# Kernel tuning notes

Hardware: AMD Instinct MI355X
Metric: run time of the kernel (lower is better)

## Reference

```python
import jax, jax.numpy as jnp
import numpy as np

B, T, D = 2, 2048, 1024
H, HKV, HD = 16, 4, 64  # num_heads, num_kv_heads, head_dim
EPS = 1.1920929e-07  # torch.finfo(float32).eps, nn.RMSNorm default


def _rmsnorm(x, g):
    return x * jax.lax.rsqrt(jnp.mean(x * x, axis=-1, keepdims=True) + EPS) * g


def _ternary(w):
    # ternary quantize {-1,0,+1} with straight-through estimator
    th = jnp.mean(jnp.abs(w))
    wt = jnp.sign(w) * (jnp.abs(w) > th).astype(w.dtype)
    return w + jax.lax.stop_gradient(wt - w)


def _bitlinear(x, w, g):
    return _rmsnorm(x, g) @ _ternary(w).T


def setup_inputs() -> dict:
    key = jax.random.key(0)
    ks = jax.random.split(key, 5)
    kaiming = lambda k, shape: jax.random.normal(k, shape, jnp.float32) * np.float32(np.sqrt(2.0 / shape[1]))
    return {
        "x": jax.random.normal(ks[0], (B, T, D), jnp.float32),
        "q_w": kaiming(ks[1], (D, D)),
        "q_g": jnp.ones((D,), jnp.float32),
        "k_w": kaiming(ks[2], (HKV * HD, D)),
        "k_g": jnp.ones((D,), jnp.float32),
        "v_w": kaiming(ks[3], (HKV * HD, D)),
        "o_w": kaiming(ks[4], (D, D)),
        "o_g": jnp.ones((D,), jnp.float32),
        "qk_gain": jnp.float32(5.25),
    }


def reference(x, q_w, q_g, k_w, k_g, v_w, o_w, o_g, qk_gain):
    b, t, d = x.shape
    q = _bitlinear(x, q_w, q_g).reshape(b, t, H, HD)          # [B,T,H,hd]
    k = _bitlinear(x, k_w, k_g).reshape(b, t, HKV, HD)        # [B,T,Hkv,hd]
    v = (x @ v_w.T).reshape(b, t, HKV, HD)                    # [B,T,Hkv,hd]
    rep = H // HKV
    k = jnp.repeat(k, rep, axis=2)                            # GQA expand -> [B,T,H,hd]
    v = jnp.repeat(v, rep, axis=2)
    scale = qk_gain / np.float32(np.sqrt(HD))
    attn = jnp.einsum('bqhd,bkhd->bhqk', q, k) * scale        # [B,H,T,T]
    causal = jnp.tril(jnp.ones((t, t), bool))
    attn = jnp.where(causal, attn, -jnp.inf)
    attn = jax.nn.softmax(attn, axis=-1)
    out = jnp.einsum('bhqk,bkhd->bqhd', attn, v).reshape(b, t, d)
    return _bitlinear(out, o_w, o_g)
```

## Files before the change

### kernel.cpp

```cpp
#include <hip/hip_runtime.h>
#include <hip/hip_bf16.h>
#include <cstdint>
#include <cstddef>

typedef unsigned short u16;
typedef unsigned int u32;
typedef __attribute__((ext_vector_type(8))) short short8v;
typedef __attribute__((ext_vector_type(4))) float f32x4;
typedef __attribute__((ext_vector_type(4))) u16 u16x4;
typedef __attribute__((ext_vector_type(8))) u16 u16x8;

static constexpr int Bc = 2, Tc = 2048, Dc = 1024, Hc = 16, HKVc = 4, HDc = 64;
static constexpr int Mc = Bc * Tc;
static constexpr float EPSc = 1.1920929e-07f;

static __device__ __forceinline__ u16 f2bf(float f) {
  u32 u = __builtin_bit_cast(u32, f);
  return (u16)((u + 0x7fffu + ((u >> 16) & 1u)) >> 16);
}
static __device__ __forceinline__ float bf2f(u16 b) {
  u32 u = ((u32)b) << 16;
  return __builtin_bit_cast(float, u);
}
static __device__ __forceinline__ float fast_exp2(float x) {
  float r;
  asm("v_exp_f32 %0, %1" : "=v"(r) : "v"(x));
  return r;
}
static __device__ __forceinline__ u32 cvt_pk_bf16(float lo, float hi) {
  u32 r;
  asm("v_cvt_pk_bf16_f32 %0, %1, %2" : "=v"(r) : "v"(lo), "v"(hi));
  return r;
}

__global__ __launch_bounds__(256) void np_leafsum_all(const float* __restrict__ q_w,
                                                      const float* __restrict__ k_w,
                                                      const float* __restrict__ o_w,
                                                      float* __restrict__ leaf) {
  int blk = blockIdx.x;
  const float* w;
  float* out;
  int lfbase;
  if (blk < 256)      { w = q_w; out = leaf;         lfbase = blk * 32; }
  else if (blk < 320) { w = k_w; out = leaf + 8192;  lfbase = (blk - 256) * 32; }
  else                { w = o_w; out = leaf + 10240; lfbase = (blk - 320) * 32; }
  int t = threadIdx.x;
  int lf = lfbase + (t >> 3), j = t & 7;
  const float* a = w + (size_t)lf * 128;
  float r = fabsf(a[j]);
#pragma unroll
  for (int i = 8; i < 128; i += 8) r += fabsf(a[i + j]);
  float x = r + __shfl_xor(r, 1);
  float y = x + __shfl_xor(x, 2);
  float z = y + __shfl_xor(y, 4);
  if (j == 0) out[lf] = z;
}

__global__ __launch_bounds__(256) void np_treemean3(const float* __restrict__ leaf,
                                                    float* __restrict__ th) {
  int m = blockIdx.x;
  const float* src = leaf + (m == 0 ? 0 : (m == 1 ? 8192 : 10240));
  int nle = (m == 1) ? 2048 : 8192;
  float inv_n = (m == 1) ? (1.0f / 262144.0f) : (1.0f / 1048576.0f);
  int t = threadIdx.x;
  int chunk = nle >> 8;
  float v[32];
  for (int i = 0; i < chunk; i += 4) {
    float4 f = *(const float4*)&src[t * chunk + i];
    v[i] = f.x; v[i + 1] = f.y; v[i + 2] = f.z; v[i + 3] = f.w;
  }
  for (int cnt = chunk >> 1; cnt >= 1; cnt >>= 1)
    for (int i = 0; i < cnt; ++i) v[i] = v[2 * i] + v[2 * i + 1];
  float s = v[0];
#pragma unroll
  for (int off = 1; off < 64; off <<= 1) s += __shfl_xor(s, off);
  __shared__ float red[4];
  if ((t & 63) == 0) red[t >> 6] = s;
  __syncthreads();
  if (t == 0) th[m] = ((red[0] + red[1]) + (red[2] + red[3])) * inv_n;
}

__global__ __launch_bounds__(256) void quant_split_all(const float* __restrict__ q_w,
                                                       const float* __restrict__ k_w,
                                                       const float* __restrict__ o_w,
                                                       const float* __restrict__ v_w,
                                                       const float* __restrict__ th,
                                                       u16* __restrict__ Wq,
                                                       u16* __restrict__ Wk,
                                                       u16* __restrict__ Wo,
                                                       u16* __restrict__ Vwh) {
  int i4 = blockIdx.x * 256 + threadIdx.x;
  if (i4 < 589824) {
    const float* w; u16* o; float t;
    int j;
    if (i4 < 262144)      { w = q_w; o = Wq; t = th[0]; j = i4; }
    else if (i4 < 327680) { w = k_w; o = Wk; t = th[1]; j = i4 - 262144; }
    else                  { w = o_w; o = Wo; t = th[2]; j = i4 - 327680; }
    float4 v = *(const float4*)&w[(size_t)j * 4];
    float y[4] = {v.x, v.y, v.z, v.w};
    u16x4 q;
#pragma unroll
    for (int c = 0; c < 4; ++c)
      q[c] = (y[c] > t) ? (u16)0x3F80 : ((y[c] < -t) ? (u16)0xBF80 : (u16)0);
    *(u16x4*)&o[(size_t)j * 4] = q;
  } else {
    int j = i4 - 589824;
    float4 v = *(const float4*)&v_w[(size_t)j * 4];
    float y[4] = {v.x, v.y, v.z, v.w};
    u16x4 h;
#pragma unroll
    for (int c = 0; c < 4; ++c) h[c] = f2bf(y[c]);
    *(u16x4*)&Vwh[(size_t)j * 4] = h;
  }
}

__global__ __launch_bounds__(256) void rmsnorm_split6(const float* __restrict__ X,
                                                      const float* __restrict__ g1,
                                                      const float* __restrict__ g2,
                                                      u16* __restrict__ H1, u16* __restrict__ L1,
                                                      u16* __restrict__ H2, u16* __restrict__ L2,
                                                      u16* __restrict__ HV) {
  int row = blockIdx.x;
  const float* xr = X + (size_t)row * Dc;
  int tid = threadIdx.x;
  float4 v = *(const float4*)&xr[tid * 4];
  float vv[4] = {v.x, v.y, v.z, v.w};
  if (HV != nullptr) {
    u16x4 h;
#pragma unroll
    for (int j = 0; j < 4; ++j) h[j] = f2bf(vv[j]);
    *(u16x4*)&HV[(size_t)row * Dc + tid * 4] = h;
  }
  float ss = v.x * v.x + v.y * v.y + v.z * v.z + v.w * v.w;
#pragma unroll
  for (int off = 1; off < 64; off <<= 1) ss += __shfl_xor(ss, off);
  __shared__ float red[4];
  if ((tid & 63) == 0) red[tid >> 6] = ss;
  __syncthreads();
  float tot = red[0] + red[1] + red[2] + red[3];
  float inv = 1.0f / sqrtf(tot * (1.0f / (float)Dc) + EPSc);
  {
    float4 a = *(const float4*)&g1[tid * 4];
    float ga[4] = {a.x, a.y, a.z, a.w};
    u16x4 h, l;
#pragma unroll
    for (int j = 0; j < 4; ++j) {
      float y = vv[j] * inv * ga[j];
      u16 hb = f2bf(y);
      h[j] = hb;
      l[j] = f2bf(y - bf2f(hb));
    }
    *(u16x4*)&H1[(size_t)row * Dc + tid * 4] = h;
    *(u16x4*)&L1[(size_t)row * Dc + tid * 4] = l;
  }
  {
    float4 a = *(const float4*)&g2[tid * 4];
    float ga[4] = {a.x, a.y, a.z, a.w};
    u16x4 h, l;
#pragma unroll
    for (int j = 0; j < 4; ++j) {
      float y = vv[j] * inv * ga[j];
      u16 hb = f2bf(y);
      h[j] = hb;
      l[j] = f2bf(y - bf2f(hb));
    }
    *(u16x4*)&H2[(size_t)row * Dc + tid * 4] = h;
    *(u16x4*)&L2[(size_t)row * Dc + tid * 4] = l;
  }
}

template <bool PA, int MODE>
static __device__ __forceinline__ void gemm_body(
    const u16* __restrict__ Ah, const u16* __restrict__ Al,
    const u16* __restrict__ Bh,
    int N, int K, int bm, int bn,
    float* __restrict__ C, u16* __restrict__ O1, u16* __restrict__ O2,
    u16* smem) {
  constexpr int APT = 2, BPT = 4;
  u16* AhS = smem;
  u16* AlS = smem + 4096;
  u16* BhS = smem + 8192;
  int tid = threadIdx.x;
  int l = tid & 63, w = tid >> 6;
  int wm = (w >> 1) * 32, wn = (w & 1) * 64;
  u16x8 rAh[APT], rAl[PA ? APT : 1], rBh[BPT];
  f32x4 acc[2][4] = {};
#define LOADTILE(kb_)                                                               \
  {                                                                                 \
    _Pragma("unroll") for (int p = 0; p < APT; ++p) {                               \
      int idx = tid + p * 256;                                                      \
      int row = idx >> 3, cc = idx & 7;                                             \
      rAh[p] = *(const u16x8*)&Ah[(size_t)(bm + row) * K + (kb_) + cc * 8];         \
      if (PA) rAl[p] = *(const u16x8*)&Al[(size_t)(bm + row) * K + (kb_) + cc * 8]; \
    }                                                                               \
    _Pragma("unroll") for (int p = 0; p < BPT; ++p) {                               \
      int idx = tid + p * 256;                                                      \
      int row = idx >> 3, cc = idx & 7;                                             \
      rBh[p] = *(const u16x8*)&Bh[(size_t)(bn + row) * K + (kb_) + cc * 8];         \
    }                                                                               \
  }
  LOADTILE(0)
  for (int kb = 0; kb < K; kb += 64) {
    __syncthreads();
#pragma unroll
    for (int p = 0; p < APT; ++p) {
      int idx = tid + p * 256;
      int row = idx >> 3, cc = idx & 7;
      int off = row * 64 + ((cc * 8) ^ ((row & 7) << 3));
      *(u16x8*)&AhS[off] = rAh[p];
      if (PA) *(u16x8*)&AlS[off] = rAl[p];
    }
#pragma unroll
    for (int p = 0; p < BPT; ++p) {
      int idx = tid + p * 256;
      int row = idx >> 3, cc = idx & 7;
      int off = row * 64 + ((cc * 8) ^ ((row & 7) << 3));
      *(u16x8*)&BhS[off] = rBh[p];
    }
    if (kb + 64 < K) LOADTILE(kb + 64)
    __syncthreads();
    __builtin_amdgcn_s_setprio(1);
#pragma unroll
    for (int sl = 0; sl < 2; ++sl) {
      short8v fa[2], fal[2], fb[4];
      int kof = (l >> 4) * 8 + sl * 32;
#pragma unroll
      for (int m = 0; m < 2; ++m) {
        int row = wm + m * 16 + (l & 15);
        int off = row * 64 + (kof ^ ((row & 7) << 3));
        fa[m] = *(const short8v*)&AhS[off];
        if (PA) fal[m] = *(const short8v*)&AlS[off];
      }
#pragma unroll
      for (int n = 0; n < 4; ++n) {
        int row = wn + n * 16 + (l & 15);
        int off = row * 64 + (kof ^ ((row & 7) << 3));
        fb[n] = *(const short8v*)&BhS[off];
      }
#pragma unroll
      for (int m = 0; m < 2; ++m)
#pragma unroll
        for (int n = 0; n < 4; ++n) {
          acc[m][n] = __builtin_amdgcn_mfma_f32_16x16x32_bf16(fa[m], fb[n], acc[m][n], 0, 0, 0);
          if (PA)
            acc[m][n] = __builtin_amdgcn_mfma_f32_16x16x32_bf16(fal[m], fb[n], acc[m][n], 0, 0, 0);
        }
    }
    __builtin_amdgcn_s_setprio(0);
  }
#undef LOADTILE
#pragma unroll
  for (int m = 0; m < 2; ++m)
#pragma unroll
    for (int n = 0; n < 4; ++n)
#pragma unroll
      for (int r = 0; r < 4; ++r) {
        int grow = bm + wm + m * 16 + (l >> 4) * 4 + r;
        int gcol = bn + wn + n * 16 + (l & 15);
        float v = acc[m][n][r];
        if (MODE == 0) {
          C[(size_t)grow * N + gcol] = v;
        } else if (MODE == 1) {
          u16 hb = f2bf(v);
          O1[(size_t)grow * N + gcol] = hb;
          O2[(size_t)grow * N + gcol] = f2bf(v - bf2f(hb));
        } else {
          int k = gcol & 31;
          int gp = (gcol & ~31) | (((k >> 2) & 3) << 3) |
                   (((k >> 4) & 1) << 2) | (k & 3);
          O1[(size_t)grow * N + gp] = f2bf(v);
        }
      }
}

__global__ __launch_bounds__(256, 1) void qkv_mega(
    const u16* __restrict__ Xqh, const u16* __restrict__ Xql, const u16* __restrict__ Wq,
    const u16* __restrict__ Xkh, const u16* __restrict__ Xkl, const u16* __restrict__ Wk,
    const u16* __restrict__ Xvh, const u16* __restrict__ Vwh,
    u16* __restrict__ Qh, u16* __restrict__ Ql,
    u16* __restrict__ Kh, u16* __restrict__ Kl,
    u16* __restrict__ Vt) {
  __shared__ __align__(16) u16 SMEM[16384];
  int bx = blockIdx.x;
  if (bx < 512) {
    int bm = (bx >> 3) * 64, bn = (bx & 7) * 128;
    gemm_body<true, 1>(Xqh, Xql, Wq, 1024, 1024, bm, bn, nullptr, Qh, Ql, SMEM);
  } else if (bx < 640) {
    int t = bx - 512;
    int bm = (t >> 1) * 64, bn = (t & 1) * 128;
    gemm_body<true, 1>(Xkh, Xkl, Wk, 256, 1024, bm, bn, nullptr, Kh, Kl, SMEM);
  } else {
    int t = bx - 640;
    int bm = (t >> 5) * 64, bn = (t & 31) * 128;
    gemm_body<false, 3>(Vwh, nullptr, Xvh, 4096, 1024, bm, bn, nullptr, Vt, nullptr, SMEM);
  }
}

__global__ __launch_bounds__(256, 1) void o_gemm(
    const u16* __restrict__ Ah, const u16* __restrict__ Bh,
    float* __restrict__ C) {
  __shared__ __align__(16) u16 SMEM[16384];
  int bm = blockIdx.y * 64, bn = blockIdx.x * 128;
  gemm_body<false, 0>(Ah, nullptr, Bh, 1024, 1024, bm, bn, C, nullptr, nullptr, SMEM);
}

__global__ __launch_bounds__(256, 3) void attn_part(
    const u16* __restrict__ Qh, const u16* __restrict__ Ql,
    const u16* __restrict__ Kh, const u16* __restrict__ Kl,
    const u16* __restrict__ Vt,
    const float* __restrict__ qk_gain,
    u16* __restrict__ Opart, float* __restrict__ MLpart) {
  __shared__ __align__(16) u16 SM[24576];
  int tid = threadIdx.x;
  int w = tid >> 6, l = tid & 63;
  int hb = blockIdx.x;
  int h = hb & 15, b = hb >> 4;
  int kvh = h >> 2;
  int f = blockIdx.y;
  int qt, s0, s1;
  if (f < 16) {
    qt = 15 - (f >> 1);
    int half = qt + 1;
    s0 = (f & 1) * half;
    s1 = s0 + half;
  } else {
    qt = 23 - f;
    s0 = 0;
    s1 = 2 * qt + 2;
  }
  int q0 = qt * 128;
  const float sc2 = qk_gain[0] * 0.125f * 1.44269504f;
  u16x8 pk[2], pl[2], pv[2];
#define AISSUE3(K0)                                                             \
  {                                                                             \
    _Pragma("unroll") for (int p = 0; p < 2; ++p) {                             \
      int idx = tid + p * 256;                                                  \
      int jj = idx >> 3, cc = idx & 7;                                          \
      size_t kb = ((size_t)(b * Tc + (K0) + jj)) * (HKVc * HDc) + kvh * 64 + cc * 8; \
      pk[p] = *(const u16x8*)&Kh[kb];                                           \
      pl[p] = *(const u16x8*)&Kl[kb];                                           \
      size_t vb = ((size_t)(kvh * 64 + jj)) * (size_t)Mc + b * Tc + (K0) + cc * 8; \
      pv[p] = *(const u16x8*)&Vt[vb];                                           \
    }                                                                           \
  }
#define WRITEBUF(BI)                                                            \
  {                                                                             \
    u16* bb = SM + (BI) * 12288;                                                \
    _Pragma("unroll") for (int p = 0; p < 2; ++p) {                             \
      int idx = tid + p * 256;                                                  \
      int jj = idx >> 3, cc = idx & 7;                                          \
      int sw = jj * 64 + ((cc * 8) ^ ((jj & 7) << 3));                          \
      *(u16x8*)&bb[sw] = pk[p];                                                 \
      *(u16x8*)&bb[4096 + sw] = pl[p];                                          \
      *(u16x8*)&bb[8192 + sw] = pv[p];                                          \
    }                                                                           \
  }
  short8v qb_h[4], qb_l[4];
#pragma unroll
  for (int qp = 0; qp < 2; ++qp) {
    size_t qrow = (size_t)(b * Tc + q0 + w * 32 + qp * 16 + (l & 15));
#pragma unroll
    for (int sl = 0; sl < 2; ++sl) {
      int dstart = (l >> 4) * 8 + sl * 32;
      qb_h[qp * 2 + sl] = *(const short8v*)&Qh[qrow * Dc + h * 64 + dstart];
      qb_l[qp * 2 + sl] = *(const short8v*)&Ql[qrow * Dc + h * 64 + dstart];
    }
  }
  f32x4 Oacc[8] = {{0,0,0,0},{0,0,0,0},{0,0,0,0},{0,0,0,0},
                   {0,0,0,0},{0,0,0,0},{0,0,0,0},{0,0,0,0}};
  float mrow[2] = {-3.0e38f, -3.0e38f};
  float lrow[2] = {0.f, 0.f};
  int qmax_w = q0 + w * 32 + 31;
  AISSUE3(s0 * 64)
  WRITEBUF(0)
  if (s0 + 1 < s1) AISSUE3((s0 + 1) * 64)
  __syncthreads();
  for (int li = 0; li < s1 - s0; ++li) {
    int stp = s0 + li;
    int k0 = stp * 64;
    u16* Kh_s = SM + (li & 1) * 12288;
    u16* Kl_s = Kh_s + 4096;
    u16* Vt_s = Kh_s + 8192;
    if (stp + 1 < s1) WRITEBUF((li + 1) & 1)
    if (stp + 2 < s1) AISSUE3((stp + 2) * 64)
    if (k0 <= qmax_w) {
      f32x4 s[8] = {{0,0,0,0},{0,0,0,0},{0,0,0,0},{0,0,0,0},
                    {0,0,0,0},{0,0,0,0},{0,0,0,0},{0,0,0,0}};
      __builtin_amdgcn_s_setprio(1);
#pragma unroll
      for (int kt = 0; kt < 4; ++kt) {
        int key = kt * 16 + (l & 15);
#pragma unroll
        for (int sl = 0; sl < 2; ++sl) {
          int dstart = ((l >> 4) * 8 + 32 * sl) ^ ((key & 7) << 3);
          short8v bh = *(const short8v*)&Kh_s[key * 64 + dstart];
          short8v bl = *(const short8v*)&Kl_s[key * 64 + dstart];
#pragma unroll
          for (int qp = 0; qp < 2; ++qp) {
            s[qp * 4 + kt] = __builtin_amdgcn_mfma_f32_16x16x32_bf16(bh, qb_h[qp * 2 + sl], s[qp * 4 + kt], 0, 0, 0);
            s[qp * 4 + kt] = __builtin_amdgcn_mfma_f32_16x16x32_bf16(bl, qb_h[qp * 2 + sl], s[qp * 4 + kt], 0, 0, 0);
            s[qp * 4 + kt] = __builtin_amdgcn_mfma_f32_16x16x32_bf16(bh, qb_l[qp * 2 + sl], s[qp * 4 + kt], 0, 0, 0);
          }
        }
      }
      __builtin_amdgcn_s_setprio(0);
      bool full = (k0 + 63) <= (q0 + w * 32);
      if (!full) {
#pragma unroll
        for (int qp = 0; qp < 2; ++qp) {
          int qg = q0 + w * 32 + qp * 16 + (l & 15);
#pragma unroll
          for (int kt = 0; kt < 4; ++kt)
#pragma unroll
            for (int r = 0; r < 4; ++r)
              if (k0 + kt * 16 + ((l >> 4) << 2) + r > qg) s[qp * 4 + kt][r] = -3.0e38f;
        }
      }
      float p[2][4][4];
#pragma unroll
      for (int qp = 0; qp < 2; ++qp) {
        float mk[4];
#pragma unroll
        for (int kt = 0; kt < 4; ++kt)
          mk[kt] = fmaxf(fmaxf(s[qp * 4 + kt][0], s[qp * 4 + kt][1]),
                         fmaxf(s[qp * 4 + kt][2], s[qp * 4 + kt][3]));
        float mx = fmaxf(fmaxf(mk[0], mk[1]), fmaxf(mk[2], mk[3]));
        mx = fmaxf(mx, __shfl_xor(mx, 16));
        mx = fmaxf(mx, __shfl_xor(mx, 32));
        float mnew = fmaxf(mrow[qp], mx);
        float msc = mnew * sc2;
        float corr = fast_exp2(__builtin_fmaf(mrow[qp], sc2, -msc));
        mrow[qp] = mnew;
        float sk[4];
#pragma unroll
        for (int kt = 0; kt < 4; ++kt) {
#pragma unroll
          for (int r = 0; r < 4; ++r)
            p[qp][kt][r] = fast_exp2(__builtin_fmaf(s[qp * 4 + kt][r], sc2, -msc));
          sk[kt] = (p[qp][kt][0] + p[qp][kt][1]) + (p[qp][kt][2] + p[qp][kt][3]);
        }
        float rs = (sk[0] + sk[1]) + (sk[2] + sk[3]);
        rs += __shfl_xor(rs, 16);
        rs += __shfl_xor(rs, 32);
        lrow[qp] = lrow[qp] * corr + rs;
#pragma unroll
        for (int dt = 0; dt < 4; ++dt) Oacc[qp * 4 + dt] *= corr;
      }
      short8v fbv[4];
#pragma unroll
      for (int qp = 0; qp < 2; ++qp)
#pragma unroll
        for (int sl = 0; sl < 2; ++sl) {
          union { u32 u[4]; short8v v; } fq;
          fq.u[0] = cvt_pk_bf16(p[qp][2 * sl][0], p[qp][2 * sl][1]);
          fq.u[1] = cvt_pk_bf16(p[qp][2 * sl][2], p[qp][2 * sl][3]);
          fq.u[2] = cvt_pk_bf16(p[qp][2 * sl + 1][0], p[qp][2 * sl + 1][1]);
          fq.u[3] = cvt_pk_bf16(p[qp][2 * sl + 1][2], p[qp][2 * sl + 1][3]);
          fbv[qp * 2 + sl] = fq.v;
        }
      __builtin_amdgcn_s_setprio(1);
#pragma unroll
      for (int dt = 0; dt < 4; ++dt) {
        int d = dt * 16 + (l & 15);
#pragma unroll
        for (int sl = 0; sl < 2; ++sl) {
          int kstart = ((l >> 4) * 8 + 32 * sl) ^ ((d & 7) << 3);
          short8v fav = *(const short8v*)&Vt_s[d * 64 + kstart];
#pragma unroll
          for (int qp = 0; qp < 2; ++qp)
            Oacc[qp * 4 + dt] = __builtin_amdgcn_mfma_f32_16x16x32_bf16(fav, fbv[qp * 2 + sl], Oacc[qp * 4 + dt], 0, 0, 0);
        }
      }
      __builtin_amdgcn_s_setprio(0);
    }
    __syncthreads();
  }
  int G = hb * 24 + f;
  u16* Op = Opart + (size_t)G * 8192;
  float* Es = (float*)SM + w * 1088;
#pragma unroll
  for (int qp = 0; qp < 2; ++qp) {
#pragma unroll
    for (int dt = 0; dt < 4; ++dt)
#pragma unroll
      for (int r = 0; r < 4; ++r)
        Es[(l & 15) * 68 + dt * 16 + ((l >> 4) << 2) + r] = Oacc[qp * 4 + dt][r];
    int qloc = w * 32 + qp * 16 + (l >> 2);
#pragma unroll
    for (int j = 0; j < 4; ++j) {
      float4 vv = *(const float4*)&Es[(l >> 2) * 68 + (l & 3) * 4 + j * 16];
      u16x4 o4;
      o4[0] = f2bf(vv.x); o4[1] = f2bf(vv.y); o4[2] = f2bf(vv.z); o4[3] = f2bf(vv.w);
      *(u16x4*)&Op[qloc * 64 + (l & 3) * 4 + j * 16] = o4;
    }
  }
  if (l < 16) {
#pragma unroll
    for (int qp = 0; qp < 2; ++qp) {
      int qloc = w * 32 + qp * 16 + l;
      MLpart[(size_t)G * 256 + qloc * 2 + 0] = mrow[qp];
      MLpart[(size_t)G * 256 + qloc * 2 + 1] = lrow[qp];
    }
  }
#undef AISSUE3
#undef WRITEBUF
}

__global__ __launch_bounds__(256) void merge_rms(const u16* __restrict__ Opart,
                                                 const float* __restrict__ MLpart,
                                                 const float* __restrict__ o_g,
                                                 const float* __restrict__ qk_gain,
                                                 u16* __restrict__ Xoh) {
  const float sc2 = qk_gain[0] * 0.125f * 1.44269504f;
  int t = threadIdx.x;
  int row_i = t >> 6, l = t & 63;
  int rr = blockIdx.x * 4 + row_i;
  int b = rr >> 11, tpos = rr & 2047;
  int qt = tpos >> 7, qloc = tpos & 127;
  int head = l >> 2;
  int hb = b * 16 + head;
  int f0, nc;
  if (qt >= 8) { f0 = 2 * (15 - qt); nc = 2; }
  else         { f0 = 23 - qt;       nc = 1; }
  size_t Gbase = (size_t)hb * 24 + f0;
  float m0 = MLpart[Gbase * 256 + qloc * 2 + 0];
  float l0 = MLpart[Gbase * 256 + qloc * 2 + 1];
  float m1 = -3.0e38f, l1 = 0.0f;
  if (nc == 2) {
    m1 = MLpart[(Gbase + 1) * 256 + qloc * 2 + 0];
    l1 = MLpart[(Gbase + 1) * 256 + qloc * 2 + 1];
  }
  float M = fmaxf(m0, m1);
  float w0 = fast_exp2((m0 - M) * sc2);
  float w1 = (nc == 2) ? fast_exp2((m1 - M) * sc2) : 0.0f;
  float L = w0 * l0 + w1 * l1;
  int dio = (l & 3) * 16;
  const u16* Op0 = Opart + Gbase * 8192 + qloc * 64 + dio;
  float val[16];
  {
    u16x8 a0 = *(const u16x8*)&Op0[0];
    u16x8 a1 = *(const u16x8*)&Op0[8];
#pragma unroll
    for (int j = 0; j < 8; ++j) { val[j] = w0 * bf2f(a0[j]); val[8 + j] = w0 * bf2f(a1[j]); }
  }
  if (nc == 2) {
    const u16* Op1 = Op0 + 8192;
    u16x8 a0 = *(const u16x8*)&Op1[0];
    u16x8 a1 = *(const u16x8*)&Op1[8];
#pragma unroll
    for (int j = 0; j < 8; ++j) { val[j] += w1 * bf2f(a0[j]); val[8 + j] += w1 * bf2f(a1[j]); }
  }
  float invL = 1.0f / L;
#pragma unroll
  for (int j = 0; j < 16; ++j) val[j] *= invL;
  float ss = 0.0f;
#pragma unroll
  for (int j = 0; j < 16; ++j) ss += val[j] * val[j];
#pragma unroll
  for (int off = 1; off < 64; off <<= 1) ss += __shfl_xor(ss, off);
  float inv = 1.0f / sqrtf(ss * (1.0f / (float)Dc) + EPSc);
  int col = head * 64 + dio;
  u16x8 h0, h1;
#pragma unroll
  for (int j = 0; j < 8; ++j) {
    h0[j] = f2bf(val[j] * inv * o_g[col + j]);
    h1[j] = f2bf(val[8 + j] * inv * o_g[col + 8 + j]);
  }
  u16* dst = Xoh + (size_t)rr * Dc + col;
  *(u16x8*)&dst[0] = h0;
  *(u16x8*)&dst[8] = h1;
}

extern "C" void kernel_launch(void* const* d_in, const int* in_sizes, int n_in,
                              void* d_out, int out_size, void* d_ws, size_t ws_size,
                              hipStream_t stream) {
  const float* x    = (const float*)d_in[0];
  const float* q_w  = (const float*)d_in[1];
  const float* q_g  = (const float*)d_in[2];
  const float* k_w  = (const float*)d_in[3];
  const float* k_g  = (const float*)d_in[4];
  const float* v_w  = (const float*)d_in[5];
  const float* o_w  = (const float*)d_in[6];
  const float* o_g  = (const float*)d_in[7];
  const float* qk_g = (const float*)d_in[8];

  char* base = (char*)d_ws;
  u16* Xqh = (u16*)(base + (0ull  << 20));
  u16* Xql = (u16*)(base + (8ull  << 20));
  u16* Xkh = (u16*)(base + (16ull << 20));
  u16* Xkl = (u16*)(base + (24ull << 20));
  u16* Xvh = (u16*)(base + (32ull << 20));
  u16* Qh  = (u16*)(base + (40ull << 20));
  u16* Ql  = (u16*)(base + (48ull << 20));
  u16* Kh  = (u16*)(base + (56ull << 20));
  u16* Kl  = (u16*)(base + (58ull << 20));
  u16* Vt  = (u16*)(base + (60ull << 20));
  u16* Wq  = (u16*)(base + (62ull << 20));
  u16* Wk  = (u16*)(base + (64ull << 20));
  u16* Wo  = (u16*)(base + (64ull << 20) + (512ull << 10));
  u16* Vwh = (u16*)(base + (66ull << 20) + (512ull << 10));
  float* leaf = (float*)(base + (67ull << 20));
  float* th   = leaf + 18432;
  u16*  Opart   = (u16*)(base + (16ull << 20));
  float* MLpart = (float*)(base + (28ull << 20));
  u16*  Xoh     = (u16*)base;

  np_leafsum_all<<<576, 256, 0, stream>>>(q_w, k_w, o_w, leaf);
  np_treemean3<<<3, 256, 0, stream>>>(leaf, th);

  quant_split_all<<<2560, 256, 0, stream>>>(q_w, k_w, o_w, v_w, th, Wq, Wk, Wo, Vwh);

  rmsnorm_split6<<<Mc, 256, 0, stream>>>(x, q_g, k_g, Xqh, Xql, Xkh, Xkl, Xvh);

  qkv_mega<<<768, 256, 0, stream>>>(Xqh, Xql, Wq, Xkh, Xkl, Wk, Xvh, Vwh,
                                    Qh, Ql, Kh, Kl, Vt);

  attn_part<<<dim3(32, 24), 256, 0, stream>>>(Qh, Ql, Kh, Kl, Vt, qk_g, Opart, MLpart);

  merge_rms<<<1024, 256, 0, stream>>>(Opart, MLpart, o_g, qk_g, Xoh);

  o_gemm<<<dim3(8, 64), 256, 0, stream>>>(Xoh, Wo, (float*)d_out);
}
```

Measured before the change: 133.3 us.

## Enlarge attention Q tile to 256 rows with table-driven split-K schedule

Each attention block now covers 256 query rows instead of 128, with each wave handling 64 rows. Every K/V tile loaded into shared memory is therefore reused by twice as many queries. The work split across 16 blocks per head comes from constant lookup tables that balance the causal workload, and a query tile can now be split into up to three partial chunks that merge_rms combines. The cost is more accumulator registers per thread (occupancy hint drops from 3 to 2) and fewer blocks in the grid.

```diff
diff --git a/kernel.cpp b/kernel.cpp
--- a/kernel.cpp
+++ b/kernel.cpp
@@ -13,6 +13,12 @@
 static constexpr int Bc = 2, Tc = 2048, Dc = 1024, Hc = 16, HKVc = 4, HDc = 64;
 static constexpr int Mc = Bc * Tc;
 static constexpr float EPSc = 1.1920929e-07f;
+
+__constant__ int C_FQT[16] = {5,5,2,7,7,7,6,4, 1,1,0,3,3,6,6,4};
+__constant__ int C_FS0[16] = {0,12,0,0,11,22,0,0, 0,4,0,0,8,10,19,10};
+__constant__ int C_FNS[16] = {12,12,12,11,11,10,10,10, 4,4,4,8,8,9,9,10};
+__constant__ int C_NC[8]   = {1,2,1,2,2,2,3,3};
+__constant__ int C_FL[24]  = {10,0,0, 8,9,0, 2,0,0, 11,12,0, 7,15,0, 0,1,0, 6,13,14, 3,4,5};
 
 static __device__ __forceinline__ u16 f2bf(float f) {
   u32 u = __builtin_bit_cast(u32, f);
@@ -304,7 +310,7 @@
   gemm_body<false, 0>(Ah, nullptr, Bh, 1024, 1024, bm, bn, C, nullptr, nullptr, SMEM);
 }
 
-__global__ __launch_bounds__(256, 3) void attn_part(
+__global__ __launch_bounds__(256, 2) void attn_part(
     const u16* __restrict__ Qh, const u16* __restrict__ Ql,
     const u16* __restrict__ Kh, const u16* __restrict__ Kl,
     const u16* __restrict__ Vt,
@@ -317,18 +323,10 @@
   int h = hb & 15, b = hb >> 4;
   int kvh = h >> 2;
   int f = blockIdx.y;
-  int qt, s0, s1;
-  if (f < 16) {
-    qt = 15 - (f >> 1);
-    int half = qt + 1;
-    s0 = (f & 1) * half;
-    s1 = s0 + half;
-  } else {
-    qt = 23 - f;
-    s0 = 0;
-    s1 = 2 * qt + 2;
-  }
-  int q0 = qt * 128;
+  int qt = C_FQT[f];
+  int s0 = C_FS0[f];
+  int s1 = s0 + C_FNS[f];
+  int q0 = qt * 256;
   const float sc2 = qk_gain[0] * 0.125f * 1.44269504f;
   u16x8 pk[2], pl[2], pv[2];
 #define AISSUE3(K0)                                                             \
@@ -355,10 +353,10 @@
       *(u16x8*)&bb[8192 + sw] = pv[p];                                          \
     }                                                                           \
   }
-  short8v qb_h[4], qb_l[4];
-#pragma unroll
-  for (int qp = 0; qp < 2; ++qp) {
-    size_t qrow = (size_t)(b * Tc + q0 + w * 32 + qp * 16 + (l & 15));
+  short8v qb_h[8], qb_l[8];
+#pragma unroll
+  for (int qp = 0; qp < 4; ++qp) {
+    size_t qrow = (size_t)(b * Tc + q0 + w * 64 + qp * 16 + (l & 15));
 #pragma unroll
     for (int sl = 0; sl < 2; ++sl) {
       int dstart = (l >> 4) * 8 + sl * 32;
@@ -366,11 +364,10 @@
       qb_l[qp * 2 + sl] = *(const short8v*)&Ql[qrow * Dc + h * 64 + dstart];
     }
   }
-  f32x4 Oacc[8] = {{0,0,0,0},{0,0,0,0},{0,0,0,0},{0,0,0,0},
-                   {0,0,0,0},{0,0,0,0},{0,0,0,0},{0,0,0,0}};
-  float mrow[2] = {-3.0e38f, -3.0e38f};
-  float lrow[2] = {0.f, 0.f};
-  int qmax_w = q0 + w * 32 + 31;
+  f32x4 Oacc[16] = {};
+  float mrow[4] = {-3.0e38f, -3.0e38f, -3.0e38f, -3.0e38f};
+  float lrow[4] = {0.f, 0.f, 0.f, 0.f};
+  int qmax_w = q0 + w * 64 + 63;
   AISSUE3(s0 * 64)
   WRITEBUF(0)
   if (s0 + 1 < s1) AISSUE3((s0 + 1) * 64)
@@ -384,8 +381,7 @@
     if (stp + 1 < s1) WRITEBUF((li + 1) & 1)
     if (stp + 2 < s1) AISSUE3((stp + 2) * 64)
     if (k0 <= qmax_w) {
-      f32x4 s[8] = {{0,0,0,0},{0,0,0,0},{0,0,0,0},{0,0,0,0},
-                    {0,0,0,0},{0,0,0,0},{0,0,0,0},{0,0,0,0}};
+      f32x4 s[16] = {};
       __builtin_amdgcn_s_setprio(1);
 #pragma unroll
       for (int kt = 0; kt < 4; ++kt) {
@@ -396,7 +392,7 @@
           short8v bh = *(const short8v*)&Kh_s[key * 64 + dstart];
           short8v bl = *(const short8v*)&Kl_s[key * 64 + dstart];
 #pragma unroll
-          for (int qp = 0; qp < 2; ++qp) {
+          for (int qp = 0; qp < 4; ++qp) {
             s[qp * 4 + kt] = __builtin_amdgcn_mfma_f32_16x16x32_bf16(bh, qb_h[qp * 2 + sl], s[qp * 4 + kt], 0, 0, 0);
             s[qp * 4 + kt] = __builtin_amdgcn_mfma_f32_16x16x32_bf16(bl, qb_h[qp * 2 + sl], s[qp * 4 + kt], 0, 0, 0);
             s[qp * 4 + kt] = __builtin_amdgcn_mfma_f32_16x16x32_bf16(bh, qb_l[qp * 2 + sl], s[qp * 4 + kt], 0, 0, 0);
@@ -404,11 +400,11 @@
         }
       }
       __builtin_amdgcn_s_setprio(0);
-      bool full = (k0 + 63) <= (q0 + w * 32);
+      bool full = (k0 + 63) <= (q0 + w * 64);
       if (!full) {
 #pragma unroll
-        for (int qp = 0; qp < 2; ++qp) {
-          int qg = q0 + w * 32 + qp * 16 + (l & 15);
+        for (int qp = 0; qp < 4; ++qp) {
+          int qg = q0 + w * 64 + qp * 16 + (l & 15);
 #pragma unroll
           for (int kt = 0; kt < 4; ++kt)
 #pragma unroll
@@ -416,9 +412,9 @@
               if (k0 + kt * 16 + ((l >> 4) << 2) + r > qg) s[qp * 4 + kt][r] = -3.0e38f;
         }
       }
-      float p[2][4][4];
-#pragma unroll
-      for (int qp = 0; qp < 2; ++qp) {
+      short8v fbv[8];
+#pragma unroll
+      for (int qp = 0; qp < 4; ++qp) {
         float mk[4];
 #pragma unroll
         for (int kt = 0; kt < 4; ++kt)
@@ -431,13 +427,14 @@
         float msc = mnew * sc2;
         float corr = fast_exp2(__builtin_fmaf(mrow[qp], sc2, -msc));
         mrow[qp] = mnew;
+        float p[4][4];
         float sk[4];
 #pragma unroll
         for (int kt = 0; kt < 4; ++kt) {
 #pragma unroll
           for (int r = 0; r < 4; ++r)
-            p[qp][kt][r] = fast_exp2(__builtin_fmaf(s[qp * 4 + kt][r], sc2, -msc));
-          sk[kt] = (p[qp][kt][0] + p[qp][kt][1]) + (p[qp][kt][2] + p[qp][kt][3]);
+            p[kt][r] = fast_exp2(__builtin_fmaf(s[qp * 4 + kt][r], sc2, -msc));
+          sk[kt] = (p[kt][0] + p[kt][1]) + (p[kt][2] + p[kt][3]);
         }
         float rs = (sk[0] + sk[1]) + (sk[2] + sk[3]);
         rs += __shfl_xor(rs, 16);
@@ -445,19 +442,16 @@
         lrow[qp] = lrow[qp] * corr + rs;
 #pragma unroll
         for (int dt = 0; dt < 4; ++dt) Oacc[qp * 4 + dt] *= corr;
-      }
-      short8v fbv[4];
-#pragma unroll
-      for (int qp = 0; qp < 2; ++qp)
 #pragma unroll
         for (int sl = 0; sl < 2; ++sl) {
           union { u32 u[4]; short8v v; } fq;
-          fq.u[0] = cvt_pk_bf16(p[qp][2 * sl][0], p[qp][2 * sl][1]);
-          fq.u[1] = cvt_pk_bf16(p[qp][2 * sl][2], p[qp][2 * sl][3]);
-          fq.u[2] = cvt_pk_bf16(p[qp][2 * sl + 1][0], p[qp][2 * sl + 1][1]);
-          fq.u[3] = cvt_pk_bf16(p[qp][2 * sl + 1][2], p[qp][2 * sl + 1][3]);
+          fq.u[0] = cvt_pk_bf16(p[2 * sl][0], p[2 * sl][1]);
+          fq.u[1] = cvt_pk_bf16(p[2 * sl][2], p[2 * sl][3]);
+          fq.u[2] = cvt_pk_bf16(p[2 * sl + 1][0], p[2 * sl + 1][1]);
+          fq.u[3] = cvt_pk_bf16(p[2 * sl + 1][2], p[2 * sl + 1][3]);
           fbv[qp * 2 + sl] = fq.v;
         }
+      }
       __builtin_amdgcn_s_setprio(1);
 #pragma unroll
       for (int dt = 0; dt < 4; ++dt) {
@@ -467,7 +461,7 @@
           int kstart = ((l >> 4) * 8 + 32 * sl) ^ ((d & 7) << 3);
           short8v fav = *(const short8v*)&Vt_s[d * 64 + kstart];
 #pragma unroll
-          for (int qp = 0; qp < 2; ++qp)
+          for (int qp = 0; qp < 4; ++qp)
             Oacc[qp * 4 + dt] = __builtin_amdgcn_mfma_f32_16x16x32_bf16(fav, fbv[qp * 2 + sl], Oacc[qp * 4 + dt], 0, 0, 0);
         }
       }
@@ -475,17 +469,17 @@
     }
     __syncthreads();
   }
-  int G = hb * 24 + f;
-  u16* Op = Opart + (size_t)G * 8192;
+  int G = hb * 16 + f;
+  u16* Op = Opart + (size_t)G * 16384;
   float* Es = (float*)SM + w * 1088;
 #pragma unroll
-  for (int qp = 0; qp < 2; ++qp) {
+  for (int qp = 0; qp < 4; ++qp) {
 #pragma unroll
     for (int dt = 0; dt < 4; ++dt)
 #pragma unroll
       for (int r = 0; r < 4; ++r)
         Es[(l & 15) * 68 + dt * 16 + ((l >> 4) << 2) + r] = Oacc[qp * 4 + dt][r];
-    int qloc = w * 32 + qp * 16 + (l >> 2);
+    int qloc = w * 64 + qp * 16 + (l >> 2);
 #pragma unroll
     for (int j = 0; j < 4; ++j) {
       float4 vv = *(const float4*)&Es[(l >> 2) * 68 + (l & 3) * 4 + j * 16];
@@ -496,10 +490,10 @@
   }
   if (l < 16) {
 #pragma unroll
-    for (int qp = 0; qp < 2; ++qp) {
-      int qloc = w * 32 + qp * 16 + l;
-      MLpart[(size_t)G * 256 + qloc * 2 + 0] = mrow[qp];
-      MLpart[(size_t)G * 256 + qloc * 2 + 1] = lrow[qp];
+    for (int qp = 0; qp < 4; ++qp) {
+      int qloc = w * 64 + qp * 16 + l;
+      MLpart[(size_t)G * 512 + qloc * 2 + 0] = mrow[qp];
+      MLpart[(size_t)G * 512 + qloc * 2 + 1] = lrow[qp];
     }
   }
 #undef AISSUE3
@@ -516,39 +510,30 @@
   int row_i = t >> 6, l = t & 63;
   int rr = blockIdx.x * 4 + row_i;
   int b = rr >> 11, tpos = rr & 2047;
-  int qt = tpos >> 7, qloc = tpos & 127;
+  int qt = tpos >> 8, qloc = tpos & 255;
   int head = l >> 2;
   int hb = b * 16 + head;
-  int f0, nc;
-  if (qt >= 8) { f0 = 2 * (15 - qt); nc = 2; }
-  else         { f0 = 23 - qt;       nc = 1; }
-  size_t Gbase = (size_t)hb * 24 + f0;
-  float m0 = MLpart[Gbase * 256 + qloc * 2 + 0];
-  float l0 = MLpart[Gbase * 256 + qloc * 2 + 1];
-  float m1 = -3.0e38f, l1 = 0.0f;
-  if (nc == 2) {
-    m1 = MLpart[(Gbase + 1) * 256 + qloc * 2 + 0];
-    l1 = MLpart[(Gbase + 1) * 256 + qloc * 2 + 1];
-  }
-  float M = fmaxf(m0, m1);
-  float w0 = fast_exp2((m0 - M) * sc2);
-  float w1 = (nc == 2) ? fast_exp2((m1 - M) * sc2) : 0.0f;
-  float L = w0 * l0 + w1 * l1;
+  int nc = C_NC[qt];
+  float mi[3], li_[3];
+  size_t Gi[3];
+  float M = -3.0e38f;
+  for (int i = 0; i < nc; ++i) {
+    Gi[i] = (size_t)hb * 16 + C_FL[qt * 3 + i];
+    mi[i] = MLpart[Gi[i] * 512 + qloc * 2 + 0];
+    li_[i] = MLpart[Gi[i] * 512 + qloc * 2 + 1];
+    M = fmaxf(M, mi[i]);
+  }
   int dio = (l & 3) * 16;
-  const u16* Op0 = Opart + Gbase * 8192 + qloc * 64 + dio;
-  float val[16];
-  {
-    u16x8 a0 = *(const u16x8*)&Op0[0];
-    u16x8 a1 = *(const u16x8*)&Op0[8];
-#pragma unroll
-    for (int j = 0; j < 8; ++j) { val[j] = w0 * bf2f(a0[j]); val[8 + j] = w0 * bf2f(a1[j]); }
-  }
-  if (nc == 2) {
-    const u16* Op1 = Op0 + 8192;
-    u16x8 a0 = *(const u16x8*)&Op1[0];
-    u16x8 a1 = *(const u16x8*)&Op1[8];
-#pragma unroll
-    for (int j = 0; j < 8; ++j) { val[j] += w1 * bf2f(a0[j]); val[8 + j] += w1 * bf2f(a1[j]); }
+  float val[16] = {};
+  float L = 0.0f;
+  for (int i = 0; i < nc; ++i) {
+    float wgt = fast_exp2((mi[i] - M) * sc2);
+    L += wgt * li_[i];
+    const u16* Op = Opart + Gi[i] * 16384 + qloc * 64 + dio;
+    u16x8 a0 = *(const u16x8*)&Op[0];
+    u16x8 a1 = *(const u16x8*)&Op[8];
+#pragma unroll
+    for (int j = 0; j < 8; ++j) { val[j] += wgt * bf2f(a0[j]); val[8 + j] += wgt * bf2f(a1[j]); }
   }
   float invL = 1.0f / L;
 #pragma unroll
@@ -602,7 +587,7 @@
   float* leaf = (float*)(base + (67ull << 20));
   float* th   = leaf + 18432;
   u16*  Opart   = (u16*)(base + (16ull << 20));
-  float* MLpart = (float*)(base + (28ull << 20));
+  float* MLpart = (float*)(base + (32ull << 20));
   u16*  Xoh     = (u16*)base;
 
   np_leafsum_all<<<576, 256, 0, stream>>>(q_w, k_w, o_w, leaf);
@@ -615,7 +600,7 @@
   qkv_mega<<<768, 256, 0, stream>>>(Xqh, Xql, Wq, Xkh, Xkl, Wk, Xvh, Vwh,
                                     Qh, Ql, Kh, Kl, Vt);
 
-  attn_part<<<dim3(32, 24), 256, 0, stream>>>(Qh, Ql, Kh, Kl, Vt, qk_g, Opart, MLpart);
+  attn_part<<<dim3(32, 16), 256, 0, stream>>>(Qh, Ql, Kh, Kl, Vt, qk_g, Opart, MLpart);
 
   merge_rms<<<1024, 256, 0, stream>>>(Opart, MLpart, o_g, qk_g, Xoh);
 
```

After: 140.2 us. 5.2% more time.
